# Kernel optimization log

Hardware: AMD Instinct MI355X
Metric: run time of the kernel (lower is better)

## Reference

```python
import jax, jax.numpy as jnp
import numpy as np

C_S, C_P, FEAT_DIM, NUM_BINS = 256, 128, 64, 22
TOTAL_EDGE_FEATS = FEAT_DIM * 2 + NUM_BINS * 2 + 2  # embed_diffuse_mask=True
LN_EPS = 1e-5


def calc_distogram(pos, min_bin, max_bin, num_bins):
    # pos: [B, N, 3] -> one-hot distance bins [B, N, N, num_bins]
    d = jnp.linalg.norm(pos[:, :, None, :] - pos[:, None, :, :], axis=-1)[..., None]
    lower = jnp.linspace(min_bin, max_bin, num_bins, dtype=pos.dtype)
    upper = jnp.concatenate([lower[1:], jnp.array([1e8], dtype=pos.dtype)])
    return ((d > lower) & (d < upper)).astype(pos.dtype)


def cross_concat(f):
    # f: [B, N, D] -> [B, N, N, 2D]: row-broadcast feats then col-broadcast feats
    B, N, D = f.shape
    fi = jnp.broadcast_to(f[:, :, None, :], (B, N, N, D))
    fj = jnp.broadcast_to(f[:, None, :, :], (B, N, N, D))
    return jnp.concatenate([fi, fj], axis=-1)


def setup_inputs() -> dict:
    key = jax.random.key(0)
    ks = jax.random.split(key, 12)
    B, N = 2, 512
    inp = {
        'init_node_embed': jax.random.normal(ks[0], (B, N, C_S), jnp.float32),
        'trans_t': jax.random.normal(ks[1], (B, N, 3), jnp.float32),
        'trans_sc': jax.random.normal(ks[2], (B, N, 3), jnp.float32),
        'edge_mask': jnp.ones((B, N, N), jnp.float32),
        'diffuse_mask': jnp.ones((B, N), jnp.float32),
        # params (fan-in scaled)
        'Wsp': jax.random.normal(ks[3], (C_S, FEAT_DIM), jnp.float32) / np.sqrt(C_S),
        'bsp': jnp.zeros((FEAT_DIM,), jnp.float32),
        'W1': jax.random.normal(ks[4], (TOTAL_EDGE_FEATS, C_P), jnp.float32) / np.sqrt(TOTAL_EDGE_FEATS),
        'b1': jnp.zeros((C_P,), jnp.float32),
        'W2': jax.random.normal(ks[5], (C_P, C_P), jnp.float32) / np.sqrt(C_P),
        'b2': jnp.zeros((C_P,), jnp.float32),
        'W3': jax.random.normal(ks[6], (C_P, C_P), jnp.float32) / np.sqrt(C_P),
        'b3': jnp.zeros((C_P,), jnp.float32),
        'ln_g': jnp.ones((C_P,), jnp.float32),
        'ln_b': jnp.zeros((C_P,), jnp.float32),
    }
    return inp


def reference(init_node_embed, trans_t, trans_sc, edge_mask, diffuse_mask,
              Wsp, bsp, W1, b1, W2, b2, W3, b3, ln_g, ln_b):
    p_i = init_node_embed @ Wsp + bsp                      # [B,N,feat_dim]
    cross_node = cross_concat(p_i)                          # [B,N,N,2*feat_dim]
    dist_feats = calc_distogram(trans_t, 1e-3, 20.0, NUM_BINS)
    sc_feats = calc_distogram(trans_sc, 1e-3, 20.0, NUM_BINS)
    diff_feat = cross_concat(diffuse_mask[..., None])       # [B,N,N,2]
    feats = jnp.concatenate([cross_node, dist_feats, sc_feats, diff_feat], axis=-1)
    h = jax.nn.relu(feats @ W1 + b1)
    h = jax.nn.relu(h @ W2 + b2)
    h = h @ W3 + b3
    mu = jnp.mean(h, axis=-1, keepdims=True)
    var = jnp.mean(jnp.square(h - mu), axis=-1, keepdims=True)
    h = (h - mu) * jax.lax.rsqrt(var + LN_EPS) * ln_g + ln_b
    return h * edge_mask[..., None]
```

## Files before the change

### kernel.cpp

```cpp
#include <hip/hip_runtime.h>
#include <hip/hip_bf16.h>
#include <math.h>

#define NB 2
#define NN 512
#define CS 256
#define CP 128
#define FD 64
#define NBINS 22
#define EPB 64

typedef __attribute__((ext_vector_type(8))) short bf16x8;
typedef __attribute__((ext_vector_type(4))) short bf16x4;
typedef __attribute__((ext_vector_type(4))) float f32x4;

__device__ __forceinline__ unsigned short f2bf_rne(float x) {
    unsigned int u = __float_as_uint(x);
    unsigned int r = (u + 0x7fffu + ((u >> 16) & 1u)) >> 16;
    return (unsigned short)r;
}
__device__ __forceinline__ float bf2f(unsigned short b) {
    return __uint_as_float(((unsigned int)b) << 16);
}
__device__ __forceinline__ unsigned short f2bf(float x) {
    __hip_bfloat16 h = __float2bfloat16(x);
    unsigned short u;
    __builtin_memcpy(&u, &h, 2);
    return u;
}

__device__ __forceinline__ int bin_of(float d, float step) {
    const float fk = __fdiv_rn(__fsub_rn(d, 0.001f), step);
    int k0 = (int)fk;
    k0 = k0 < 1 ? 1 : (k0 > 20 ? 20 : k0);
    int row = -1;
    #pragma unroll
    for (int dk = -1; dk <= 1; ++dk) {
        const int k = k0 + dk;
        const float lo = __fadd_rn(0.001f, __fmul_rn((float)k, step));
        const float hi = (k == NBINS - 1)
                       ? 1e8f
                       : __fadd_rn(0.001f, __fmul_rn((float)(k + 1), step));
        row = (d > lo && d < hi) ? k : row;
    }
    return row;
}

__global__ __launch_bounds__(256) void ef_prep_kernel(
    const float* __restrict__ x,
    const float* __restrict__ diffuse,
    const float* __restrict__ Wsp,
    const float* __restrict__ bsp,
    const float* __restrict__ W1,
    const float* __restrict__ b1,
    const float* __restrict__ W2,
    const float* __restrict__ W3,
    const float* __restrict__ trans_t,
    const float* __restrict__ trans_sc,
    float* __restrict__ qr,
    unsigned short* __restrict__ Wp,
    unsigned short* __restrict__ binsP)
{
    __shared__ float xs[CS];
    __shared__ float ps[FD];
    const int t = threadIdx.x;
    if (blockIdx.x < 1024) {
        const int n = blockIdx.x;
        xs[t] = x[(size_t)n * CS + t];
        __syncthreads();
        if (t < FD) {
            float acc = bsp[t];
            #pragma unroll 8
            for (int k = 0; k < CS; ++k)
                acc = fmaf(xs[k], Wsp[k * FD + t], acc);
            ps[t] = acc;
        }
        __syncthreads();
        const float dm = diffuse[n];
        const int c = t & (CP - 1);
        if (t < CP) {
            float acc = b1[c] + dm * W1[172 * CP + c];
            #pragma unroll 8
            for (int k = 0; k < FD; ++k)
                acc = fmaf(ps[k], W1[k * CP + c], acc);
            qr[(size_t)n * CP + c] = acc;
        } else {
            float acc = dm * W1[173 * CP + c];
            #pragma unroll 8
            for (int k = 0; k < FD; ++k)
                acc = fmaf(ps[k], W1[(FD + k) * CP + c], acc);
            qr[(size_t)(1024 + n) * CP + c] = acc;
        }
    } else if (blockIdx.x < 1088) {
        const int s = (blockIdx.x - 1024) * 256 + t;
        const int j    = s & 7;
        const int lane = (s >> 3) & 63;
        const int mt   = (s >> 9) & 7;
        const int ki   = s >> 12;
        const int k = 32 * ki + 8 * (lane >> 4) + j;
        const int n = 16 * mt + (lane & 15);
        Wp[s]         = f2bf_rne(W2[k * CP + n]);
        Wp[16384 + s] = f2bf_rne(W3[k * CP + n]);
    } else {
        const int e  = (blockIdx.x - 1088) * 256 + t;
        const int bb = e >> 18;
        const int ii = (e >> 9) & (NN - 1);
        const int jj = e & (NN - 1);
        const int ni = bb * NN + ii;
        const int nj = bb * NN + jj;
        const float step = __fdiv_rn(__fsub_rn(20.0f, 0.001f), 21.0f);
        float dx = __fsub_rn(trans_t[ni * 3 + 0], trans_t[nj * 3 + 0]);
        float dy = __fsub_rn(trans_t[ni * 3 + 1], trans_t[nj * 3 + 1]);
        float dz = __fsub_rn(trans_t[ni * 3 + 2], trans_t[nj * 3 + 2]);
        const float dT = sqrtf(__fadd_rn(__fadd_rn(__fmul_rn(dx, dx), __fmul_rn(dy, dy)), __fmul_rn(dz, dz)));
        dx = __fsub_rn(trans_sc[ni * 3 + 0], trans_sc[nj * 3 + 0]);
        dy = __fsub_rn(trans_sc[ni * 3 + 1], trans_sc[nj * 3 + 1]);
        dz = __fsub_rn(trans_sc[ni * 3 + 2], trans_sc[nj * 3 + 2]);
        const float dS = sqrtf(__fadd_rn(__fadd_rn(__fmul_rn(dx, dx), __fmul_rn(dy, dy)), __fmul_rn(dz, dz)));
        const int kT = bin_of(dT, step);
        const int kS = bin_of(dS, step);
        binsP[e] = (unsigned short)((unsigned int)(kT + 1) | ((unsigned int)(kS + 1) << 8));
    }
}

__global__ __launch_bounds__(256, 4) void ef_edge_kernel(
    const float* __restrict__ edge_mask,
    const float* __restrict__ W1,
    const float* __restrict__ b2,
    const float* __restrict__ b3,
    const float* __restrict__ ln_g,
    const float* __restrict__ ln_b,
    const float* __restrict__ qr,
    const unsigned short* __restrict__ Wp,
    const unsigned short* __restrict__ binsP,
    float* __restrict__ out)
{
    __shared__ unsigned short hb[8192];
    char* hb8 = (char*)hb;
    float* psum_s  = (float*)hb8;
    float* pqsum_s = (float*)(hb8 + 4352);
    float* mus     = (float*)(hb8 + 8704);
    float* invs    = (float*)(hb8 + 8960);

    const int t   = threadIdx.x;
    const int blk = blockIdx.x;
    const int jt  = blk & 7;
    const int i   = (blk >> 3) & (NN - 1);
    const int b   = blk >> 12;
    const int j0  = jt * EPB;
    const int nodeI  = b * NN + i;
    const int nodeJ0 = b * NN + j0;

    const int w  = t >> 6;
    const int l  = t & 63;
    const int lr = l & 15;
    const int lg = l >> 4;
    const int e1 = t >> 2;
    const int c0 = (t & 3) * 32;
    const int nj = nodeJ0 + e1;

    const size_t erow0 = ((size_t)(b * NN + i)) * NN + (j0 + e1);
    const unsigned int pk = binsP[erow0];
    const int kT = (int)(pk & 0xffu) - 1;
    const int kS = (int)(pk >> 8) - 1;

    {
        const float fT = (kT < 0) ? 0.0f : 1.0f;
        const float fS = (kS < 0) ? 0.0f : 1.0f;
        const float* qrow = qr + (size_t)nodeI * CP + c0;
        const float* rrow = qr + (size_t)(1024 + nj) * CP + c0;
        const float* wTr  = W1 + (size_t)(kT < 0 ? 0 : 128 + kT) * CP + c0;
        const float* wSr  = W1 + (size_t)(kS < 0 ? 0 : 150 + kS) * CP + c0;
        #pragma unroll
        for (int ch = 0; ch < 4; ++ch) {
            const int cc = ch * 8;
            const float4 qa = *(const float4*)(qrow + cc);
            const float4 qb = *(const float4*)(qrow + cc + 4);
            const float4 ra = *(const float4*)(rrow + cc);
            const float4 rb = *(const float4*)(rrow + cc + 4);
            const float4 ta = *(const float4*)(wTr + cc);
            const float4 tb = *(const float4*)(wTr + cc + 4);
            const float4 sa = *(const float4*)(wSr + cc);
            const float4 sb = *(const float4*)(wSr + cc + 4);
            float h[8];
            h[0] = fmaxf(qa.x + ra.x + fT * ta.x + fS * sa.x, 0.0f);
            h[1] = fmaxf(qa.y + ra.y + fT * ta.y + fS * sa.y, 0.0f);
            h[2] = fmaxf(qa.z + ra.z + fT * ta.z + fS * sa.z, 0.0f);
            h[3] = fmaxf(qa.w + ra.w + fT * ta.w + fS * sa.w, 0.0f);
            h[4] = fmaxf(qb.x + rb.x + fT * tb.x + fS * sb.x, 0.0f);
            h[5] = fmaxf(qb.y + rb.y + fT * tb.y + fS * sb.y, 0.0f);
            h[6] = fmaxf(qb.z + rb.z + fT * tb.z + fS * sb.z, 0.0f);
            h[7] = fmaxf(qb.w + rb.w + fT * tb.w + fS * sb.w, 0.0f);
            bf16x8 H;
            #pragma unroll
            for (int u = 0; u < 8; ++u)
                H[u] = (short)f2bf(h[u]);
            const unsigned int ad = (unsigned int)e1 * 256 +
                (((unsigned int)(2 * (c0 + cc))) ^ (((unsigned int)e1 & 7) << 4));
            *(bf16x8*)(hb8 + ad) = H;
        }
    }
    __syncthreads();

    f32x4 acc[2][4];
    #pragma unroll
    for (int mt = 0; mt < 2; ++mt) {
        const float4 bv = *(const float4*)&b2[16 * (2 * w + mt) + 4 * lg];
        #pragma unroll
        for (int nt = 0; nt < 4; ++nt) {
            acc[mt][nt][0] = bv.x; acc[mt][nt][1] = bv.y;
            acc[mt][nt][2] = bv.z; acc[mt][nt][3] = bv.w;
        }
    }
    #pragma unroll
    for (int ki = 0; ki < 4; ++ki) {
        bf16x8 ah[2];
        #pragma unroll
        for (int mt = 0; mt < 2; ++mt) {
            const size_t off = (((size_t)ki * 8 + (2 * w + mt)) * 64 + l) * 8;
            ah[mt] = *(const bf16x8*)(Wp + off);
        }
        bf16x8 bh[4];
        #pragma unroll
        for (int nt = 0; nt < 4; ++nt) {
            const int e = 16 * nt + lr;
            const unsigned int ad = (unsigned int)e * 256 +
                (((unsigned int)(64 * ki + 16 * lg)) ^ (((unsigned int)e & 7) << 4));
            bh[nt] = *(const bf16x8*)(hb8 + ad);
        }
        __builtin_amdgcn_s_setprio(1);
        #pragma unroll
        for (int mt = 0; mt < 2; ++mt)
            #pragma unroll
            for (int nt = 0; nt < 4; ++nt)
                acc[mt][nt] = __builtin_amdgcn_mfma_f32_16x16x32_bf16(ah[mt], bh[nt], acc[mt][nt], 0, 0, 0);
        __builtin_amdgcn_s_setprio(0);
    }
    __syncthreads();

    #pragma unroll
    for (int mt = 0; mt < 2; ++mt) {
        const int mtg = 2 * w + mt;
        #pragma unroll
        for (int nt = 0; nt < 4; ++nt) {
            const int e = 16 * nt + lr;
            bf16x4 H;
            H[0] = (short)f2bf(fmaxf(acc[mt][nt][0], 0.0f));
            H[1] = (short)f2bf(fmaxf(acc[mt][nt][1], 0.0f));
            H[2] = (short)f2bf(fmaxf(acc[mt][nt][2], 0.0f));
            H[3] = (short)f2bf(fmaxf(acc[mt][nt][3], 0.0f));
            const unsigned int ad = (unsigned int)e * 256 +
                (((unsigned int)(32 * mtg + 8 * lg)) ^ (((unsigned int)e & 7) << 4));
            *(bf16x4*)(hb8 + ad) = H;
        }
    }
    __syncthreads();

    #pragma unroll
    for (int mt = 0; mt < 2; ++mt) {
        const float4 bv = *(const float4*)&b3[16 * (2 * w + mt) + 4 * lg];
        #pragma unroll
        for (int nt = 0; nt < 4; ++nt) {
            acc[mt][nt][0] = bv.x; acc[mt][nt][1] = bv.y;
            acc[mt][nt][2] = bv.z; acc[mt][nt][3] = bv.w;
        }
    }
    #pragma unroll
    for (int ki = 0; ki < 4; ++ki) {
        bf16x8 ah[2];
        #pragma unroll
        for (int mt = 0; mt < 2; ++mt) {
            const size_t off = (((size_t)ki * 8 + (2 * w + mt)) * 64 + l) * 8;
            ah[mt] = *(const bf16x8*)(Wp + 16384 + off);
        }
        bf16x8 bh[4];
        #pragma unroll
        for (int nt = 0; nt < 4; ++nt) {
            const int e = 16 * nt + lr;
            const unsigned int ad = (unsigned int)e * 256 +
                (((unsigned int)(64 * ki + 16 * lg)) ^ (((unsigned int)e & 7) << 4));
            bh[nt] = *(const bf16x8*)(hb8 + ad);
        }
        __builtin_amdgcn_s_setprio(1);
        #pragma unroll
        for (int mt = 0; mt < 2; ++mt)
            #pragma unroll
            for (int nt = 0; nt < 4; ++nt)
                acc[mt][nt] = __builtin_amdgcn_mfma_f32_16x16x32_bf16(ah[mt], bh[nt], acc[mt][nt], 0, 0, 0);
        __builtin_amdgcn_s_setprio(0);
    }
    __syncthreads();

    #pragma unroll
    for (int nt = 0; nt < 4; ++nt) {
        const int e = 16 * nt + lr;
        float s = 0.0f, s2 = 0.0f;
        #pragma unroll
        for (int mt = 0; mt < 2; ++mt)
            #pragma unroll
            for (int r = 0; r < 4; ++r) {
                const float v = acc[mt][nt][r];
                s += v;
                s2 = fmaf(v, v, s2);
            }
        psum_s[e * 17 + 4 * w + lg]  = s;
        pqsum_s[e * 17 + 4 * w + lg] = s2;
    }
    __syncthreads();

    {
        const int e = t & 63;
        float s = 0.0f, s2 = 0.0f;
        #pragma unroll
        for (int k = 0; k < 16; ++k) {
            s  += psum_s[e * 17 + k];
            s2 += pqsum_s[e * 17 + k];
        }
        const float mu  = s * (1.0f / 128.0f);
        const float var = s2 * (1.0f / 128.0f) - mu * mu;
        mus[e]  = mu;
        invs[e] = rsqrtf(var + 1e-5f);
    }
    __syncthreads();

    {
        float4 g4[2], bb4[2];
        #pragma unroll
        for (int mt = 0; mt < 2; ++mt) {
            const int n0 = 16 * (2 * w + mt) + 4 * lg;
            g4[mt]  = *(const float4*)&ln_g[n0];
            bb4[mt] = *(const float4*)&ln_b[n0];
        }
        #pragma unroll
        for (int nt = 0; nt < 4; ++nt) {
            const int e = 16 * nt + lr;
            const size_t erow = ((size_t)(b * NN + i)) * NN + (j0 + e);
            const float em  = edge_mask[erow];
            const float mu  = mus[e];
            const float inv = invs[e];
            float* op = out + erow * CP;
            #pragma unroll
            for (int mt = 0; mt < 2; ++mt) {
                const int n0 = 16 * (2 * w + mt) + 4 * lg;
                float4 o;
                o.x = ((acc[mt][nt][0] - mu) * inv * g4[mt].x + bb4[mt].x) * em;
                o.y = ((acc[mt][nt][1] - mu) * inv * g4[mt].y + bb4[mt].y) * em;
                o.z = ((acc[mt][nt][2] - mu) * inv * g4[mt].z + bb4[mt].z) * em;
                o.w = ((acc[mt][nt][3] - mu) * inv * g4[mt].w + bb4[mt].w) * em;
                *(float4*)(op + n0) = o;
            }
        }
    }
}

extern "C" void kernel_launch(void* const* d_in, const int* in_sizes, int n_in,
                              void* d_out, int out_size, void* d_ws, size_t ws_size,
                              hipStream_t stream) {
    const float* init_node = (const float*)d_in[0];
    const float* trans_t   = (const float*)d_in[1];
    const float* trans_sc  = (const float*)d_in[2];
    const float* edge_mask = (const float*)d_in[3];
    const float* diffuse   = (const float*)d_in[4];
    const float* Wsp       = (const float*)d_in[5];
    const float* bsp       = (const float*)d_in[6];
    const float* W1        = (const float*)d_in[7];
    const float* b1        = (const float*)d_in[8];
    const float* W2        = (const float*)d_in[9];
    const float* b2        = (const float*)d_in[10];
    const float* W3        = (const float*)d_in[11];
    const float* b3        = (const float*)d_in[12];
    const float* ln_g      = (const float*)d_in[13];
    const float* ln_b      = (const float*)d_in[14];
    float* out = (float*)d_out;
    float* qr  = (float*)d_ws;
    unsigned short* Wp    = (unsigned short*)((char*)d_ws + (1 << 20));
    unsigned short* binsP = (unsigned short*)((char*)d_ws + (1 << 20) + 65536);

    ef_prep_kernel<<<1024 + 64 + 2048, 256, 0, stream>>>(
        init_node, diffuse, Wsp, bsp, W1, b1, W2, W3, trans_t, trans_sc,
        qr, Wp, binsP);
    ef_edge_kernel<<<NB * NN * (NN / EPB), 256, 0, stream>>>(
        edge_mask, W1, b2, b3, ln_g, ln_b, qr, Wp, binsP, out);
}
```

Before: 186.8 us.

## Double edge tile to 128 per block with 512 threads, one M-tile per wave

Each block now processes 128 edges with 8 waves instead of 64 edges with 4 waves. Each wave owns one 16-row output-channel tile and loops over 8 edge tiles, so it loads a single A fragment per k-step rather than two. LDS use grows to about 34 KB and the LayerNorm partial-sum reduction widens to 32 partials per edge. The hidden layer-1 section is not shown, so it is unclear whether that code was adapted to 512 threads and 128 edges. Fewer blocks also halves the grid size.

```diff
diff --git a/kernel.cpp b/kernel.cpp
--- a/kernel.cpp
+++ b/kernel.cpp
@@ -8,7 +8,7 @@
 #define CP 128
 #define FD 64
 #define NBINS 22
-#define EPB 64
+#define EPB 128
 
 typedef __attribute__((ext_vector_type(8))) short bf16x8;
 typedef __attribute__((ext_vector_type(4))) short bf16x4;
@@ -123,7 +123,7 @@
     }
 }
 
-__global__ __launch_bounds__(256, 4) void ef_edge_kernel(
+__global__ __launch_bounds__(512, 4) void ef_edge_kernel(
     const float* __restrict__ edge_mask,
     const float* __restrict__ W1,
     const float* __restrict__ b2,
@@ -135,18 +135,18 @@
     const unsigned short* __restrict__ binsP,
     float* __restrict__ out)
 {
-    __shared__ unsigned short hb[8192];
-    char* hb8 = (char*)hb;
-    float* psum_s  = (float*)hb8;
-    float* pqsum_s = (float*)(hb8 + 4352);
-    float* mus     = (float*)(hb8 + 8704);
-    float* invs    = (float*)(hb8 + 8960);
+    __shared__ char slab[34816];
+    char* hb8 = slab;
+    float* psum_s  = (float*)slab;
+    float* pqsum_s = (float*)(slab + 16896);
+    float* mus     = (float*)(slab + 33792);
+    float* invs    = (float*)(slab + 34304);
 
     const int t   = threadIdx.x;
     const int blk = blockIdx.x;
-    const int jt  = blk & 7;
-    const int i   = (blk >> 3) & (NN - 1);
-    const int b   = blk >> 12;
+    const int jt  = blk & 3;
+    const int i   = (blk >> 2) & (NN - 1);
+    const int b   = blk >> 11;
     const int j0  = jt * EPB;
     const int nodeI  = b * NN + i;
     const int nodeJ0 = b * NN + j0;
@@ -202,27 +202,22 @@
     }
     __syncthreads();
 
-    f32x4 acc[2][4];
-    #pragma unroll
-    for (int mt = 0; mt < 2; ++mt) {
-        const float4 bv = *(const float4*)&b2[16 * (2 * w + mt) + 4 * lg];
-        #pragma unroll
-        for (int nt = 0; nt < 4; ++nt) {
-            acc[mt][nt][0] = bv.x; acc[mt][nt][1] = bv.y;
-            acc[mt][nt][2] = bv.z; acc[mt][nt][3] = bv.w;
+    f32x4 acc[8];
+    {
+        const float4 bv = *(const float4*)&b2[16 * w + 4 * lg];
+        #pragma unroll
+        for (int nt = 0; nt < 8; ++nt) {
+            acc[nt][0] = bv.x; acc[nt][1] = bv.y;
+            acc[nt][2] = bv.z; acc[nt][3] = bv.w;
         }
     }
     #pragma unroll
     for (int ki = 0; ki < 4; ++ki) {
-        bf16x8 ah[2];
-        #pragma unroll
-        for (int mt = 0; mt < 2; ++mt) {
-            const size_t off = (((size_t)ki * 8 + (2 * w + mt)) * 64 + l) * 8;
-            ah[mt] = *(const bf16x8*)(Wp + off);
-        }
-        bf16x8 bh[4];
-        #pragma unroll
-        for (int nt = 0; nt < 4; ++nt) {
+        const size_t aoff = (((size_t)ki * 8 + w) * 64 + l) * 8;
+        const bf16x8 ah = *(const bf16x8*)(Wp + aoff);
+        bf16x8 bh[8];
+        #pragma unroll
+        for (int nt = 0; nt < 8; ++nt) {
             const int e = 16 * nt + lr;
             const unsigned int ad = (unsigned int)e * 256 +
                 (((unsigned int)(64 * ki + 16 * lg)) ^ (((unsigned int)e & 7) << 4));
@@ -230,52 +225,41 @@
         }
         __builtin_amdgcn_s_setprio(1);
         #pragma unroll
-        for (int mt = 0; mt < 2; ++mt)
-            #pragma unroll
-            for (int nt = 0; nt < 4; ++nt)
-                acc[mt][nt] = __builtin_amdgcn_mfma_f32_16x16x32_bf16(ah[mt], bh[nt], acc[mt][nt], 0, 0, 0);
+        for (int nt = 0; nt < 8; ++nt)
+            acc[nt] = __builtin_amdgcn_mfma_f32_16x16x32_bf16(ah, bh[nt], acc[nt], 0, 0, 0);
         __builtin_amdgcn_s_setprio(0);
     }
     __syncthreads();
 
     #pragma unroll
-    for (int mt = 0; mt < 2; ++mt) {
-        const int mtg = 2 * w + mt;
-        #pragma unroll
-        for (int nt = 0; nt < 4; ++nt) {
-            const int e = 16 * nt + lr;
-            bf16x4 H;
-            H[0] = (short)f2bf(fmaxf(acc[mt][nt][0], 0.0f));
-            H[1] = (short)f2bf(fmaxf(acc[mt][nt][1], 0.0f));
-            H[2] = (short)f2bf(fmaxf(acc[mt][nt][2], 0.0f));
-            H[3] = (short)f2bf(fmaxf(acc[mt][nt][3], 0.0f));
-            const unsigned int ad = (unsigned int)e * 256 +
-                (((unsigned int)(32 * mtg + 8 * lg)) ^ (((unsigned int)e & 7) << 4));
-            *(bf16x4*)(hb8 + ad) = H;
-        }
-    }
-    __syncthreads();
-
-    #pragma unroll
-    for (int mt = 0; mt < 2; ++mt) {
-        const float4 bv = *(const float4*)&b3[16 * (2 * w + mt) + 4 * lg];
-        #pragma unroll
-        for (int nt = 0; nt < 4; ++nt) {
-            acc[mt][nt][0] = bv.x; acc[mt][nt][1] = bv.y;
-            acc[mt][nt][2] = bv.z; acc[mt][nt][3] = bv.w;
+    for (int nt = 0; nt < 8; ++nt) {
+        const int e = 16 * nt + lr;
+        bf16x4 H;
+        H[0] = (short)f2bf(fmaxf(acc[nt][0], 0.0f));
+        H[1] = (short)f2bf(fmaxf(acc[nt][1], 0.0f));
+        H[2] = (short)f2bf(fmaxf(acc[nt][2], 0.0f));
+        H[3] = (short)f2bf(fmaxf(acc[nt][3], 0.0f));
+        const unsigned int ad = (unsigned int)e * 256 +
+            (((unsigned int)(32 * w + 8 * lg)) ^ (((unsigned int)e & 7) << 4));
+        *(bf16x4*)(hb8 + ad) = H;
+    }
+    __syncthreads();
+
+    {
+        const float4 bv = *(const float4*)&b3[16 * w + 4 * lg];
+        #pragma unroll
+        for (int nt = 0; nt < 8; ++nt) {
+            acc[nt][0] = bv.x; acc[nt][1] = bv.y;
+            acc[nt][2] = bv.z; acc[nt][3] = bv.w;
         }
     }
     #pragma unroll
     for (int ki = 0; ki < 4; ++ki) {
-        bf16x8 ah[2];
-        #pragma unroll
-        for (int mt = 0; mt < 2; ++mt) {
-            const size_t off = (((size_t)ki * 8 + (2 * w + mt)) * 64 + l) * 8;
-            ah[mt] = *(const bf16x8*)(Wp + 16384 + off);
-        }
-        bf16x8 bh[4];
-        #pragma unroll
-        for (int nt = 0; nt < 4; ++nt) {
+        const size_t aoff = (((size_t)ki * 8 + w) * 64 + l) * 8;
+        const bf16x8 ah = *(const bf16x8*)(Wp + 16384 + aoff);
+        bf16x8 bh[8];
+        #pragma unroll
+        for (int nt = 0; nt < 8; ++nt) {
             const int e = 16 * nt + lr;
             const unsigned int ad = (unsigned int)e * 256 +
                 (((unsigned int)(64 * ki + 16 * lg)) ^ (((unsigned int)e & 7) << 4));
@@ -283,38 +267,34 @@
         }
         __builtin_amdgcn_s_setprio(1);
         #pragma unroll
-        for (int mt = 0; mt < 2; ++mt)
-            #pragma unroll
-            for (int nt = 0; nt < 4; ++nt)
-                acc[mt][nt] = __builtin_amdgcn_mfma_f32_16x16x32_bf16(ah[mt], bh[nt], acc[mt][nt], 0, 0, 0);
+        for (int nt = 0; nt < 8; ++nt)
+            acc[nt] = __builtin_amdgcn_mfma_f32_16x16x32_bf16(ah, bh[nt], acc[nt], 0, 0, 0);
         __builtin_amdgcn_s_setprio(0);
     }
     __syncthreads();
 
     #pragma unroll
-    for (int nt = 0; nt < 4; ++nt) {
+    for (int nt = 0; nt < 8; ++nt) {
         const int e = 16 * nt + lr;
         float s = 0.0f, s2 = 0.0f;
         #pragma unroll
-        for (int mt = 0; mt < 2; ++mt)
-            #pragma unroll
-            for (int r = 0; r < 4; ++r) {
-                const float v = acc[mt][nt][r];
-                s += v;
-                s2 = fmaf(v, v, s2);
-            }
-        psum_s[e * 17 + 4 * w + lg]  = s;
-        pqsum_s[e * 17 + 4 * w + lg] = s2;
-    }
-    __syncthreads();
-
-    {
-        const int e = t & 63;
+        for (int r = 0; r < 4; ++r) {
+            const float v = acc[nt][r];
+            s += v;
+            s2 = fmaf(v, v, s2);
+        }
+        psum_s[e * 33 + 4 * w + lg]  = s;
+        pqsum_s[e * 33 + 4 * w + lg] = s2;
+    }
+    __syncthreads();
+
+    {
+        const int e = t & 127;
         float s = 0.0f, s2 = 0.0f;
         #pragma unroll
-        for (int k = 0; k < 16; ++k) {
-            s  += psum_s[e * 17 + k];
-            s2 += pqsum_s[e * 17 + k];
+        for (int k = 0; k < 32; ++k) {
+            s  += psum_s[e * 33 + k];
+            s2 += pqsum_s[e * 33 + k];
         }
         const float mu  = s * (1.0f / 128.0f);
         const float var = s2 * (1.0f / 128.0f) - mu * mu;
@@ -324,31 +304,22 @@
     __syncthreads();
 
     {
-        float4 g4[2], bb4[2];
-        #pragma unroll
-        for (int mt = 0; mt < 2; ++mt) {
-            const int n0 = 16 * (2 * w + mt) + 4 * lg;
-            g4[mt]  = *(const float4*)&ln_g[n0];
-            bb4[mt] = *(const float4*)&ln_b[n0];
-        }
-        #pragma unroll
-        for (int nt = 0; nt < 4; ++nt) {
+        const int n0 = 16 * w + 4 * lg;
+        const float4 g4 = *(const float4*)&ln_g[n0];
+        const float4 bb = *(const float4*)&ln_b[n0];
+        #pragma unroll
+        for (int nt = 0; nt < 8; ++nt) {
             const int e = 16 * nt + lr;
             const size_t erow = ((size_t)(b * NN + i)) * NN + (j0 + e);
             const float em  = edge_mask[erow];
             const float mu  = mus[e];
             const float inv = invs[e];
-            float* op = out + erow * CP;
-            #pragma unroll
-            for (int mt = 0; mt < 2; ++mt) {
-                const int n0 = 16 * (2 * w + mt) + 4 * lg;
-                float4 o;
-                o.x = ((acc[mt][nt][0] - mu) * inv * g4[mt].x + bb4[mt].x) * em;
-                o.y = ((acc[mt][nt][1] - mu) * inv * g4[mt].y + bb4[mt].y) * em;
-                o.z = ((acc[mt][nt][2] - mu) * inv * g4[mt].z + bb4[mt].z) * em;
-                o.w = ((acc[mt][nt][3] - mu) * inv * g4[mt].w + bb4[mt].w) * em;
-                *(float4*)(op + n0) = o;
-            }
+            float4 o;
+            o.x = ((acc[nt][0] - mu) * inv * g4.x + bb.x) * em;
+            o.y = ((acc[nt][1] - mu) * inv * g4.y + bb.y) * em;
+            o.z = ((acc[nt][2] - mu) * inv * g4.z + bb.z) * em;
+            o.w = ((acc[nt][3] - mu) * inv * g4.w + bb.w) * em;
+            *(float4*)(out + erow * CP + n0) = o;
         }
     }
 }
@@ -379,6 +350,6 @@
     ef_prep_kernel<<<1024 + 64 + 2048, 256, 0, stream>>>(
         init_node, diffuse, Wsp, bsp, W1, b1, W2, W3, trans_t, trans_sc,
         qr, Wp, binsP);
-    ef_edge_kernel<<<NB * NN * (NN / EPB), 256, 0, stream>>>(
+    ef_edge_kernel<<<NB * NN * (NN / EPB), 512, 0, stream>>>(
         edge_mask, W1, b2, b3, ln_g, ln_b, qr, Wp, binsP, out);
 }
```

Result: slower. 200.4 us (+7.3%).
